# Kernel tuning notes

Measured on AMD Instinct MI355X. Metric: run time of the kernel, lower is better.

## Reference

```python
import jax, jax.numpy as jnp
import numpy as np

RADIUS = 5.0          # cutoff radius (Angstrom)
MAX_NBR = 32          # max_num_neighbors_threshold
CELL_L = 12.0         # cubic box edge; > 2*RADIUS/2 so rep=1 (27 image cells)


def setup_inputs() -> dict:
    key = jax.random.key(0)
    k1, _ = jax.random.split(key)
    B, N = 16, 256
    pos = jax.random.uniform(k1, (B, N, 3), dtype=jnp.float32) * CELL_L
    cell = jnp.tile(jnp.eye(3, dtype=jnp.float32)[None] * CELL_L, (B, 1, 1))
    return {"pos": pos, "cell": cell}


def reference(pos, cell):
    # pos: [B,N,3] atom positions, cell: [B,3,3] lattice vectors (rows a1,a2,a3)
    B, N, _ = pos.shape
    # periodic image offsets n in {-1,0,1}^3 -> unit: [C,3], C=27
    r = jnp.arange(-1, 2, dtype=pos.dtype)
    n1, n2, n3 = jnp.meshgrid(r, r, r, indexing="ij")
    unit = jnp.stack([n1.ravel(), n2.ravel(), n3.ravel()], axis=-1)  # [C,3]
    C = unit.shape[0]
    # pbc_offsets[b,c,:] = sum_k n_k * a_k  (== bmm(cell^T, unit^T) in torch code)
    offsets = jnp.einsum("ck,bkd->bcd", unit, cell)  # [B,C,3]
    # candidate edge vectors: receiver i, source j shifted by image offset c
    dvec = pos[:, :, None, None, :] - (pos[:, None, :, None, :] + offsets[:, None, None, :, :])  # [B,N,N,C,3]
    dsqr = jnp.sum(dvec * dvec, axis=-1)  # [B,N,N,C]
    # radius mask + remove self (atom_distance_sqr > 1e-4)
    within = (dsqr <= RADIUS * RADIUS) & (dsqr > 1e-4)
    M = N * C
    dsqr_f = jnp.where(within, dsqr, jnp.inf).reshape(B, N, M)
    # per-receiver sort-based top-K truncation (mirrors get_max_neighbors_mask:
    # index_copy into [num_atoms, max_nbr] padded with inf, sort, keep first K finite)
    order = jnp.argsort(dsqr_f, axis=-1)
    rank = jnp.argsort(order, axis=-1)           # rank of each candidate among its receiver's neighbors
    keep = (rank < MAX_NBR) & jnp.isfinite(dsqr_f)  # [B,N,M] final edge mask
    dist = jnp.where(keep, jnp.sqrt(jnp.where(keep, dsqr_f, 1.0)), 0.0)  # masked edge lengths
    dvec_m = jnp.where(keep[..., None], dvec.reshape(B, N, M, 3), 0.0)   # masked edge vectors
    # num_neighbors_image == segment_csr(clamp(num_neighbors, K)) == per-image kept-edge count
    num_neighbors_image = jnp.sum(keep.reshape(B, -1), axis=-1).astype(jnp.int32)
    return dist, dvec_m, num_neighbors_image
```

## Files before the change

kernel.cpp:

```cpp
#include <hip/hip_runtime.h>
#include <stdint.h>


constexpr int B_ = 16, N_ = 256, C_ = 27;
constexpr int M_ = N_ * C_;
constexpr int G_ = M_ / 4;
constexpr int MAXC = 1024;
constexpr int KMAX = 32;

__global__ __launch_bounds__(256)
void nbr_kernel(const float* __restrict__ pos,
                const float* __restrict__ cell,
                float* __restrict__ dist,
                float* __restrict__ dvec,
                float* __restrict__ nn)
{
#pragma clang fp contract(off)
    __shared__ float ps[N_ * 3];
    __shared__ float offs[C_ * 3];
    __shared__ unsigned long long keys[MAXC];
    __shared__ int cnt;
    __shared__ unsigned long long tau_s;

    const int bi  = blockIdx.x;
    const int b   = bi >> 8;
    const int i   = bi & 255;
    const int tid = threadIdx.x;

    const float* pb = pos + b * N_ * 3;
    for (int t = tid; t < N_ * 3; t += 256) ps[t] = pb[t];
    if (tid < C_) {
        const float n1 = (float)(tid / 9 - 1);
        const float n2 = (float)((tid / 3) % 3 - 1);
        const float n3 = (float)(tid % 3 - 1);
        const float* cb = cell + b * 9;
        for (int d = 0; d < 3; ++d)
            offs[tid * 3 + d] = n1 * cb[d] + n2 * cb[3 + d] + n3 * cb[6 + d];
    }
    if (tid == 0) { cnt = 0; tau_s = ~0ULL; }
    __syncthreads();

    const float pix = ps[i * 3 + 0], piy = ps[i * 3 + 1], piz = ps[i * 3 + 2];

    for (int k = 0; k < C_; ++k) {
        const int m = tid + (k << 8);
        const int j = m / C_;
        const int c = m - j * C_;
        const float sx = ps[j * 3 + 0] + offs[c * 3 + 0];
        const float sy = ps[j * 3 + 1] + offs[c * 3 + 1];
        const float sz = ps[j * 3 + 2] + offs[c * 3 + 2];
        const float dx = pix - sx, dy = piy - sy, dz = piz - sz;
        const float dsq = dx * dx + dy * dy + dz * dz;
        if (dsq <= 25.0f && dsq > 1e-4f) {
            const int idx = atomicAdd(&cnt, 1);
            if (idx < MAXC)
                keys[idx] = ((unsigned long long)__float_as_uint(dsq) << 32) | (unsigned)m;
        }
    }
    __syncthreads();

    int K = cnt; if (K > MAXC) K = MAXC;
    for (int idx = tid; idx < K; idx += 256) {
        const unsigned long long key = keys[idx];
        int r = 0;
        for (int q = 0; q < K; ++q) r += (keys[q] < key) ? 1 : 0;
        if (r == KMAX - 1) tau_s = key;
    }
    __syncthreads();

    if (tid == 0)
        atomicAdd(&nn[b], (float)(K < KMAX ? K : KMAX));

    const unsigned long long tau = tau_s;
    float* __restrict__ drow = dist + (size_t)bi * M_;
    float* __restrict__ vrow = dvec + (size_t)bi * (size_t)(M_ * 3);

    for (int g = tid; g < G_; g += 256) {
        const int m0 = g * 4;
        float dv[4], vv[12];
        #pragma unroll
        for (int u = 0; u < 4; ++u) {
            const int m = m0 + u;
            const int j = m / C_;
            const int c = m - j * C_;
            const float sx = ps[j * 3 + 0] + offs[c * 3 + 0];
            const float sy = ps[j * 3 + 1] + offs[c * 3 + 1];
            const float sz = ps[j * 3 + 2] + offs[c * 3 + 2];
            const float dx = pix - sx, dy = piy - sy, dz = piz - sz;
            const float dsq = dx * dx + dy * dy + dz * dz;
            const bool within = (dsq <= 25.0f) && (dsq > 1e-4f);
            const unsigned long long key =
                ((unsigned long long)__float_as_uint(dsq) << 32) | (unsigned)m;
            const bool keep = within && (key <= tau);
            dv[u]         = keep ? sqrtf(dsq) : 0.0f;
            vv[u * 3 + 0] = keep ? dx : 0.0f;
            vv[u * 3 + 1] = keep ? dy : 0.0f;
            vv[u * 3 + 2] = keep ? dz : 0.0f;
        }
        *(float4*)(drow + m0) = make_float4(dv[0], dv[1], dv[2], dv[3]);
        float4* vp = (float4*)(vrow + (size_t)m0 * 3);
        vp[0] = make_float4(vv[0], vv[1], vv[2],  vv[3]);
        vp[1] = make_float4(vv[4], vv[5], vv[6],  vv[7]);
        vp[2] = make_float4(vv[8], vv[9], vv[10], vv[11]);
    }
}

extern "C" void kernel_launch(void* const* d_in, const int* in_sizes, int n_in,
                              void* d_out, int out_size, void* d_ws, size_t ws_size,
                              hipStream_t stream)
{
    const float* pos  = (const float*)d_in[0];
    const float* cell = (const float*)d_in[1];
    float* dist = (float*)d_out;
    float* dvec = dist + (size_t)B_ * N_ * M_;
    float* nn   = dvec + (size_t)B_ * N_ * M_ * 3;
    hipMemsetAsync(nn, 0, B_ * sizeof(float), stream);
    nbr_kernel<<<dim3(B_ * N_), dim3(256), 0, stream>>>(pos, cell, dist, dvec, nn);
}
```

Before: 487.3 us.

## Zero-fill output rows and scatter only kept neighbors instead of recomputing all candidates

The second pass no longer recomputes distances for every candidate with a division-based index. Each row is streamed to zero with float4 stores, and only the top-K candidates are scattered, using dx/dy/dz/dsq cached in shared memory during the first pass. Each thread now owns one source atom and loops over the 27 images with positions held in registers, and the candidate buffer shrinks from 1024 to 256. The risks are scattered uncoalesced writes, zero-fill and scatter stores to the same addresses ordered only by a barrier, and silent truncation if a receiver ever has more than 256 in-radius candidates.

```diff
diff --git a/kernel.cpp b/kernel.cpp
--- a/kernel.cpp
+++ b/kernel.cpp
@@ -4,8 +4,7 @@
 
 constexpr int B_ = 16, N_ = 256, C_ = 27;
 constexpr int M_ = N_ * C_;
-constexpr int G_ = M_ / 4;
-constexpr int MAXC = 1024;
+constexpr int MAXC = 256;
 constexpr int KMAX = 32;
 
 __global__ __launch_bounds__(256)
@@ -16,11 +15,10 @@
                 float* __restrict__ nn)
 {
 #pragma clang fp contract(off)
-    __shared__ float ps[N_ * 3];
-    __shared__ float offs[C_ * 3];
+    __shared__ float offx[C_], offy[C_], offz[C_];
     __shared__ unsigned long long keys[MAXC];
+    __shared__ float4 vals[MAXC];
     __shared__ int cnt;
-    __shared__ unsigned long long tau_s;
 
     const int bi  = blockIdx.x;
     const int b   = bi >> 8;
@@ -28,80 +26,64 @@
     const int tid = threadIdx.x;
 
     const float* pb = pos + b * N_ * 3;
-    for (int t = tid; t < N_ * 3; t += 256) ps[t] = pb[t];
+    const float pjx = pb[tid * 3 + 0], pjy = pb[tid * 3 + 1], pjz = pb[tid * 3 + 2];
+    const float pix = pb[i * 3 + 0], piy = pb[i * 3 + 1], piz = pb[i * 3 + 2];
+
     if (tid < C_) {
         const float n1 = (float)(tid / 9 - 1);
         const float n2 = (float)((tid / 3) % 3 - 1);
         const float n3 = (float)(tid % 3 - 1);
         const float* cb = cell + b * 9;
-        for (int d = 0; d < 3; ++d)
-            offs[tid * 3 + d] = n1 * cb[d] + n2 * cb[3 + d] + n3 * cb[6 + d];
+        offx[tid] = n1 * cb[0] + n2 * cb[3] + n3 * cb[6];
+        offy[tid] = n1 * cb[1] + n2 * cb[4] + n3 * cb[7];
+        offz[tid] = n1 * cb[2] + n2 * cb[5] + n3 * cb[8];
     }
-    if (tid == 0) { cnt = 0; tau_s = ~0ULL; }
+    if (tid == 0) cnt = 0;
     __syncthreads();
 
-    const float pix = ps[i * 3 + 0], piy = ps[i * 3 + 1], piz = ps[i * 3 + 2];
+    float* __restrict__ drow = dist + (size_t)bi * M_;
+    float* __restrict__ vrow = dvec + (size_t)bi * (size_t)(M_ * 3);
 
-    for (int k = 0; k < C_; ++k) {
-        const int m = tid + (k << 8);
-        const int j = m / C_;
-        const int c = m - j * C_;
-        const float sx = ps[j * 3 + 0] + offs[c * 3 + 0];
-        const float sy = ps[j * 3 + 1] + offs[c * 3 + 1];
-        const float sz = ps[j * 3 + 2] + offs[c * 3 + 2];
+    {
+        const float4 z = make_float4(0.f, 0.f, 0.f, 0.f);
+        float4* dp = (float4*)drow;
+        float4* vp = (float4*)vrow;
+        for (int t = tid; t < M_ / 4; t += 256) dp[t] = z;
+        for (int t = tid; t < 3 * M_ / 4; t += 256) vp[t] = z;
+    }
+
+    #pragma unroll 1
+    for (int c = 0; c < C_; ++c) {
+        const float sx = pjx + offx[c], sy = pjy + offy[c], sz = pjz + offz[c];
         const float dx = pix - sx, dy = piy - sy, dz = piz - sz;
         const float dsq = dx * dx + dy * dy + dz * dz;
         if (dsq <= 25.0f && dsq > 1e-4f) {
             const int idx = atomicAdd(&cnt, 1);
-            if (idx < MAXC)
-                keys[idx] = ((unsigned long long)__float_as_uint(dsq) << 32) | (unsigned)m;
+            if (idx < MAXC) {
+                keys[idx] = ((unsigned long long)__float_as_uint(dsq) << 32)
+                          | (unsigned)(tid * C_ + c);
+                vals[idx] = make_float4(dx, dy, dz, dsq);
+            }
         }
     }
     __syncthreads();
 
     int K = cnt; if (K > MAXC) K = MAXC;
+    if (tid == 0)
+        atomicAdd(&nn[b], (float)(K < KMAX ? K : KMAX));
+
     for (int idx = tid; idx < K; idx += 256) {
         const unsigned long long key = keys[idx];
         int r = 0;
         for (int q = 0; q < K; ++q) r += (keys[q] < key) ? 1 : 0;
-        if (r == KMAX - 1) tau_s = key;
-    }
-    __syncthreads();
-
-    if (tid == 0)
-        atomicAdd(&nn[b], (float)(K < KMAX ? K : KMAX));
-
-    const unsigned long long tau = tau_s;
-    float* __restrict__ drow = dist + (size_t)bi * M_;
-    float* __restrict__ vrow = dvec + (size_t)bi * (size_t)(M_ * 3);
-
-    for (int g = tid; g < G_; g += 256) {
-        const int m0 = g * 4;
-        float dv[4], vv[12];
-        #pragma unroll
-        for (int u = 0; u < 4; ++u) {
-            const int m = m0 + u;
-            const int j = m / C_;
-            const int c = m - j * C_;
-            const float sx = ps[j * 3 + 0] + offs[c * 3 + 0];
-            const float sy = ps[j * 3 + 1] + offs[c * 3 + 1];
-            const float sz = ps[j * 3 + 2] + offs[c * 3 + 2];
-            const float dx = pix - sx, dy = piy - sy, dz = piz - sz;
-            const float dsq = dx * dx + dy * dy + dz * dz;
-            const bool within = (dsq <= 25.0f) && (dsq > 1e-4f);
-            const unsigned long long key =
-                ((unsigned long long)__float_as_uint(dsq) << 32) | (unsigned)m;
-            const bool keep = within && (key <= tau);
-            dv[u]         = keep ? sqrtf(dsq) : 0.0f;
-            vv[u * 3 + 0] = keep ? dx : 0.0f;
-            vv[u * 3 + 1] = keep ? dy : 0.0f;
-            vv[u * 3 + 2] = keep ? dz : 0.0f;
+        if (r < KMAX) {
+            const int m = (int)(key & 0xffffffffu);
+            const float4 v = vals[idx];
+            drow[m]         = sqrtf(v.w);
+            vrow[m * 3 + 0] = v.x;
+            vrow[m * 3 + 1] = v.y;
+            vrow[m * 3 + 2] = v.z;
         }
-        *(float4*)(drow + m0) = make_float4(dv[0], dv[1], dv[2], dv[3]);
-        float4* vp = (float4*)(vrow + (size_t)m0 * 3);
-        vp[0] = make_float4(vv[0], vv[1], vv[2],  vv[3]);
-        vp[1] = make_float4(vv[4], vv[5], vv[6],  vv[7]);
-        vp[2] = make_float4(vv[8], vv[9], vv[10], vv[11]);
     }
 }
 
```

Measured after the change: 472.3 us. 1.03x faster.
